# Optimization experiments

Hardware: AMD Instinct MI355X
Metric: run time of the kernel (lower is better)

The kernel has to match this reference:

```python
import jax, jax.numpy as jnp
import numpy as np

# ---- constants mirroring init_kwargs ----
S = 128          # sheet_units
KA = 25          # aff_cf_units
C = 2            # aff_cf_channels
KL = 25          # lat_cf_units
EXC = 9          # exc_units
DA = 1           # aff_cf_dilation
DL = 1           # lat_cf_dilation
HOMEO_TARGET = 0.04
STRENGTH = 1.0

# ---- radial helper masks (get_circle / get_radial_cos) ----
def _dist(n):
    g = jnp.arange(n, dtype=jnp.float32) - (n - 1) / 2.0
    return jnp.sqrt(g[:, None] ** 2 + g[None, :] ** 2)

def _circle(n, r):
    return (_dist(n) < r).astype(jnp.float32)

def _rcos(n, wl):
    return jnp.cos(_dist(n) * jnp.pi / wl)

# afferent envelope: [C*KA*KA], channel-major like torch repeat+view
_ae = _rcos(KA, KA) ** 2 * _circle(KA, KA / 2)
_ae = _ae / _ae.max()
AFF_ENV = jnp.tile(_ae.reshape(1, KA * KA), (C, 1)).reshape(C * KA * KA)

# lateral (LRI) envelope: [KL*KL]
_inh = _rcos(KL, EXC / DL) ** 2 * _circle(KL, EXC / (2 * DL))
_le = _rcos(KL, KL) ** 2 * (1.0 - _inh) * _circle(KL, KL / 2)
LRI_ENV = (_le / _le.max()).reshape(KL * KL)

def _unfold(x, k, dil):
    """x: [C,H,W] -> patches [L, C*k*k], torch F.unfold ordering (C slowest)."""
    Cc, H, W = x.shape
    out = H - dil * (k - 1)
    idx = jnp.arange(out)[:, None] + dil * jnp.arange(k)[None, :]  # [out,k]
    p = x[:, idx, :]          # [C,out,k,W]
    p = p[:, :, :, idx]       # [C,out,k,out,k]
    p = p.transpose(1, 3, 0, 2, 4)  # [out_i,out_j,C,ki,kj]
    return p.reshape(out * out, Cc * k * k)

def setup_inputs() -> dict:
    key = jax.random.key(0)
    k1, k2 = jax.random.split(key)
    in_size = S + DA * (KA - 1)  # 152
    x = jax.random.uniform(k1, (1, C, in_size, in_size), dtype=jnp.float32)
    rfs = jax.random.uniform(k2, (S * S, C * KA * KA, 1), dtype=jnp.float32)
    rfs = rfs / rfs.sum(1, keepdims=True)
    lat_weights = jnp.ones((S * S, KL * KL, 1), jnp.float32) / (KL * KL)
    adathresh = jnp.zeros((1, 1, S, S), jnp.float32)
    return {"x": x, "rfs": rfs, "lat_weights": lat_weights, "adathresh": adathresh}

def _forward(x, rfs, lat_weights, adathresh):
    relu = jax.nn.relu
    rfs = relu(rfs)                 # no_grad positive clamp of params
    lw = relu(lat_weights)
    # afferent: unfold + envelope + per-pixel dot (bmm with [L,F,1])
    tiles = _unfold(x[0], KA, DA) * AFF_ENV[None, :]          # [L, C*KA*KA]
    raw_aff = jnp.einsum('lf,lf->l', tiles, rfs[:, :, 0]).reshape(S, S)
    aff = jax.lax.stop_gradient(raw_aff) - adathresh[0, 0]
    lat = relu(aff)
    # lateral inhibition: pad so unfold yields S*S positions
    p = DL * (KL - 1) // 2
    lt = _unfold(jnp.pad(lat, p)[None], KL, DL) * LRI_ENV[None, :]  # [L, KL*KL]
    lat_neg = jnp.einsum('lf,lf->l', lt, jax.lax.stop_gradient(lw)[:, :, 0]).reshape(S, S)
    lat = lat - lat_neg
    lat = jnp.tanh(relu(lat * STRENGTH + aff))
    # hebbian lateral correlations term (learning_flag path)
    lt2 = _unfold(jnp.pad(lat, p, constant_values=HOMEO_TARGET)[None], KL, DL) * LRI_ENV[None, :]
    weighted = lt2 * lat.reshape(S * S, 1)
    lat_correlations = jnp.einsum('lf,lf->', weighted, lw[:, :, 0])
    return (raw_aff.reshape(1, 1, S, S), lat.reshape(1, 1, S, S),
            lat_correlations, tiles[:, None, :])

def reference(x, rfs, lat_weights, adathresh):
    return _forward(x, rfs, lat_weights, adathresh)
```

## Files before the change

kernel.cpp:

```cpp
#include <hip/hip_runtime.h>
#include <math.h>

#define S 128
#define KA 25
#define KL 25
#define PATCH 625
#define FEAT 1250
#define PI_F 3.14159265358979323846f
#define PADW 152
#define PADA (PADW * PADW)

#define WS_LRI 0
#define WS_AE 640
#define WS_LAT0P 1280
#define WS_LATFP 24384
#define WS_PART 47488
#define NPART 2048

__device__ __forceinline__ int div25(int r) { return (r * 10486) >> 18; }

__device__ __forceinline__ int woff(int r) { return r + 127 * div25(r); }

__global__ __launch_bounds__(256) void k_init(float* __restrict__ ws) {
    const int tid = threadIdx.x;
    if (blockIdx.x == 0) {
        __shared__ float s_tmp[640];
        __shared__ float s_red[4];
        for (int s = tid; s < 640; s += 256) {
            int q = s / 160;
            int t = s - q * 160;
            int r = (t << 2) | q;
            float v = 0.0f;
            if (r < PATCH) {
                float di = (float)div25(r) - 12.0f;
                float dj = (float)(r - 25 * div25(r)) - 12.0f;
                float d = sqrtf(di * di + dj * dj);
                if (d < 12.5f) {
                    float c = cosf(d * (PI_F / 25.0f));
                    v = c * c;
                }
            }
            ws[WS_AE + s] = v;
        }
        float m = 0.0f;
        for (int s = tid; s < 640; s += 256) {
            int q = s / 160;
            int t = s - q * 160;
            int r = (t << 2) | q;
            float v = 0.0f;
            if (r < PATCH) {
                float di = (float)div25(r) - 12.0f;
                float dj = (float)(r - 25 * div25(r)) - 12.0f;
                float d = sqrtf(di * di + dj * dj);
                if (d < 12.5f) {
                    float c1 = cosf(d * (PI_F / 25.0f));
                    float inh = 0.0f;
                    if (d < 4.5f) {
                        float c2 = cosf(d * (PI_F / 9.0f));
                        inh = c2 * c2;
                    }
                    v = c1 * c1 * (1.0f - inh);
                }
            }
            s_tmp[s] = v;
            m = fmaxf(m, v);
        }
        for (int o = 32; o; o >>= 1) m = fmaxf(m, __shfl_down(m, o));
        if (!(tid & 63)) s_red[tid >> 6] = m;
        __syncthreads();
        float inv = 1.0f / fmaxf(fmaxf(s_red[0], s_red[1]),
                                 fmaxf(s_red[2], s_red[3]));
        for (int s = tid; s < 640; s += 256) ws[WS_LRI + s] = s_tmp[s] * inv;
    }
    const int gid = blockIdx.x * 256 + tid;
    const int gsz = gridDim.x * 256;
    for (int i = gid; i < 2 * PADA; i += gsz) {
        if (i < PADA) ws[WS_LAT0P + i] = 0.0f;
        else          ws[WS_LATFP + i - PADA] = 0.04f;
    }
}

__global__ __launch_bounds__(256) void k_aff(const float* __restrict__ x,
                                             const float* __restrict__ rfs,
                                             const float* __restrict__ ada,
                                             float* __restrict__ raw_aff,
                                             float* __restrict__ ws) {
    __shared__ float s_ae[640];
    const int tid = threadIdx.x;
    for (int i = tid; i < 640; i += 256) s_ae[i] = ws[WS_AE + i];
    __syncthreads();

    const int lane = tid & 63;
    const int wid = blockIdx.x * 4 + (tid >> 6);

    for (int l = wid; l < S * S; l += 8192) {
        const int li = l >> 7, lj = l & 127;
        const int wbase = li * PADW + lj;
        const long base = (long)l * FEAT;
        const int peel = (l & 1) ? 2 : 0;

        float acc = 0.0f;
        if (lane < peel) {
            int f = lane;
            float t = x[wbase + f] * s_ae[(f & 3) * 160 + (f >> 2)];
            acc += t * fmaxf(rfs[base + f], 0.0f);
        }
        const int n4 = (FEAT - peel) >> 2;
        for (int k = lane; k < n4; k += 64) {
            int f0 = peel + (k << 2);
            const float4 rv = *reinterpret_cast<const float4*>(rfs + base + f0);
#pragma unroll
            for (int j = 0; j < 4; ++j) {
                int f = f0 + j;
                int c = (f >= PATCH);
                int r = f - (c ? PATCH : 0);
                float t = x[c * PADA + wbase + woff(r)]
                          * s_ae[(r & 3) * 160 + (r >> 2)];
                acc += t * fmaxf((&rv.x)[j], 0.0f);
            }
        }
        const int tail = (FEAT - peel) & 3;
        if (lane < tail) {
            int f = peel + (n4 << 2) + lane;
            int r = f - PATCH;
            float t = x[PADA + wbase + woff(r)] * s_ae[(r & 3) * 160 + (r >> 2)];
            acc += t * fmaxf(rfs[base + f], 0.0f);
        }

        for (int o = 32; o; o >>= 1) acc += __shfl_down(acc, o);
        if (!lane) {
            raw_aff[l] = acc;
            ws[WS_LAT0P + (li + 12) * PADW + (lj + 12)] =
                fmaxf(acc - ada[l], 0.0f);
        }
    }
}

#define NTILE 20480000
#define NF4 5119999
__global__ __launch_bounds__(256) void k_tiles(const float* __restrict__ x,
                                               float* __restrict__ tiles,
                                               const float* __restrict__ ws) {
    __shared__ float s_ae[640];
    const int tid = threadIdx.x;
    for (int i = tid; i < 640; i += 256) s_ae[i] = ws[WS_AE + i];
    __syncthreads();

    const int gid = blockIdx.x * 256 + tid;
    const int gsz = gridDim.x * 256;
    for (long k = gid; k < NF4; k += gsz) {
        long i0 = 3 + (k << 2);
        float4 v;
#pragma unroll
        for (int j = 0; j < 4; ++j) {
            unsigned int e = (unsigned int)(i0 + j);
            unsigned int l = e / 1250u;
            int f = (int)(e - l * 1250u);
            int c = (f >= PATCH);
            int r = f - (c ? PATCH : 0);
            int li = (int)(l >> 7), lj = (int)(l & 127u);
            (&v.x)[j] = x[c * PADA + li * PADW + lj + woff(r)]
                        * s_ae[(r & 3) * 160 + (r >> 2)];
        }
        *reinterpret_cast<float4*>(tiles + i0) = v;
    }
    if (blockIdx.x == 0 && tid < 4) {
        unsigned int e = (tid < 3) ? (unsigned int)tid : (NTILE - 1u);
        unsigned int l = e / 1250u;
        int f = (int)(e - l * 1250u);
        int c = (f >= PATCH);
        int r = f - (c ? PATCH : 0);
        int li = (int)(l >> 7), lj = (int)(l & 127u);
        tiles[e] = x[c * PADA + li * PADW + lj + woff(r)]
                   * s_ae[(r & 3) * 160 + (r >> 2)];
    }
}

__global__ __launch_bounds__(256) void k_lat(const float* __restrict__ raw_aff,
                                             const float* __restrict__ ada,
                                             const float* __restrict__ lw,
                                             float* __restrict__ latf,
                                             float* __restrict__ ws) {
    __shared__ float s_le[640];
    const int tid = threadIdx.x;
    for (int i = tid; i < 640; i += 256) s_le[i] = ws[WS_LRI + i];
    __syncthreads();

    const int lane = tid & 63;
    const int wid = blockIdx.x * 4 + (tid >> 6);
    const float* __restrict__ plat0 = ws + WS_LAT0P;

    for (int l = wid; l < S * S; l += 8192) {
        const int li = l >> 7, lj = l & 127;
        const int wbase = li * PADW + lj;
        const long base = (long)l * PATCH;

        float acc = 0.0f;
        const int peel = (4 - (l & 3)) & 3;
        if (lane < peel) {
            int f = lane;
            acc += plat0[wbase + f] * s_le[(f & 3) * 160 + (f >> 2)]
                   * fmaxf(lw[base + f], 0.0f);
        }
        const int n4 = (PATCH - peel) >> 2;
        for (int k = lane; k < n4; k += 64) {
            int f0 = peel + (k << 2);
            const float4 w4 = *reinterpret_cast<const float4*>(lw + base + f0);
#pragma unroll
            for (int j = 0; j < 4; ++j) {
                int f = f0 + j;
                acc += plat0[wbase + woff(f)] * s_le[(f & 3) * 160 + (f >> 2)]
                       * fmaxf((&w4.x)[j], 0.0f);
            }
        }
        const int tail = (PATCH - peel) & 3;
        if (lane < tail) {
            int f = peel + (n4 << 2) + lane;
            acc += plat0[wbase + woff(f)] * s_le[(f & 3) * 160 + (f >> 2)]
                   * fmaxf(lw[base + f], 0.0f);
        }
        for (int o = 32; o; o >>= 1) acc += __shfl_down(acc, o);

        if (!lane) {
            float aff_l = raw_aff[l] - ada[l];
            float lat0_l = fmaxf(aff_l, 0.0f);
            float v = (lat0_l - acc)  + aff_l;
            float lv = tanhf(fmaxf(v, 0.0f));
            latf[l] = lv;
            ws[WS_LATFP + (li + 12) * PADW + (lj + 12)] = lv;
        }
    }
}

__global__ __launch_bounds__(256) void k_corr(const float* __restrict__ latf,
                                              const float* __restrict__ lw,
                                              float* __restrict__ ws) {
    __shared__ float s_le[640];
    __shared__ float s_part[4];
    const int tid = threadIdx.x;
    for (int i = tid; i < 640; i += 256) s_le[i] = ws[WS_LRI + i];
    __syncthreads();

    const int lane = tid & 63, wv = tid >> 6;
    const int wid = blockIdx.x * 4 + wv;
    const float* __restrict__ platf = ws + WS_LATFP;

    float wsum = 0.0f;
    for (int l = wid; l < S * S; l += 8192) {
        const int li = l >> 7, lj = l & 127;
        const int wbase = li * PADW + lj;
        const long base = (long)l * PATCH;

        float acc = 0.0f;
        const int peel = (4 - (l & 3)) & 3;
        if (lane < peel) {
            int f = lane;
            acc += platf[wbase + f] * s_le[(f & 3) * 160 + (f >> 2)]
                   * fmaxf(lw[base + f], 0.0f);
        }
        const int n4 = (PATCH - peel) >> 2;
        for (int k = lane; k < n4; k += 64) {
            int f0 = peel + (k << 2);
            const float4 w4 = *reinterpret_cast<const float4*>(lw + base + f0);
#pragma unroll
            for (int j = 0; j < 4; ++j) {
                int f = f0 + j;
                acc += platf[wbase + woff(f)] * s_le[(f & 3) * 160 + (f >> 2)]
                       * fmaxf((&w4.x)[j], 0.0f);
            }
        }
        const int tail = (PATCH - peel) & 3;
        if (lane < tail) {
            int f = peel + (n4 << 2) + lane;
            acc += platf[wbase + woff(f)] * s_le[(f & 3) * 160 + (f >> 2)]
                   * fmaxf(lw[base + f], 0.0f);
        }
        for (int o = 32; o; o >>= 1) acc += __shfl_down(acc, o);
        if (!lane) wsum += acc * latf[l];
    }
    if (!lane) s_part[wv] = wsum;
    __syncthreads();
    if (!tid)
        ws[WS_PART + blockIdx.x] = s_part[0] + s_part[1] + s_part[2] + s_part[3];
}

__global__ __launch_bounds__(256) void k_reduce(const float* __restrict__ ws,
                                                float* __restrict__ corr) {
    __shared__ float s_part[4];
    const int tid = threadIdx.x;
    const int lane = tid & 63, wv = tid >> 6;
    float acc = 0.0f;
    for (int i = tid; i < NPART; i += 256) acc += ws[WS_PART + i];
    for (int o = 32; o; o >>= 1) acc += __shfl_down(acc, o);
    if (!lane) s_part[wv] = acc;
    __syncthreads();
    if (!tid) corr[0] = s_part[0] + s_part[1] + s_part[2] + s_part[3];
}

extern "C" void kernel_launch(void* const* d_in, const int* in_sizes, int n_in,
                              void* d_out, int out_size, void* d_ws, size_t ws_size,
                              hipStream_t stream) {
    const float* x   = (const float*)d_in[0];
    const float* rfs = (const float*)d_in[1];
    const float* lw  = (const float*)d_in[2];
    const float* ada = (const float*)d_in[3];

    float* out      = (float*)d_out;
    float* raw_aff  = out;
    float* latf     = out + S * S;
    float* corr     = out + 2 * S * S;
    float* tiles    = out + 2 * S * S + 1;
    float* ws       = (float*)d_ws;

    k_init<<<16, 256, 0, stream>>>(ws);
    k_aff<<<2048, 256, 0, stream>>>(x, rfs, ada, raw_aff, ws);
    k_tiles<<<2048, 256, 0, stream>>>(x, tiles, ws);
    k_lat<<<2048, 256, 0, stream>>>(raw_aff, ada, lw, latf, ws);
    k_corr<<<2048, 256, 0, stream>>>(latf, lw, ws);
    k_reduce<<<1, 256, 0, stream>>>(ws, corr);
}
```

Baseline: 232.5 us.

## Fuse afferent dot and tiles output, one pixel per wave with upfront loads

Merges the afferent dot-product kernel and the tiles-materialisation kernel, so each wave computes its pixel's patch values once, writes them to the tiles output, and accumulates the dot product. This removes a second pass that recomputed every gather of x and envelope multiply. The lateral and correlation kernels also drop their grid-stride loops: each wave handles exactly one pixel and issues all its weight float4 loads before consuming them, which raises memory-level parallelism. The grid doubles to 4096 blocks and the partial-sum count grows to match. Tile stores are now scalar per element rather than float4, which could cost some write efficiency.

```diff
diff --git a/kernel.cpp b/kernel.cpp
--- a/kernel.cpp
+++ b/kernel.cpp
@@ -3,7 +3,6 @@
 
 #define S 128
 #define KA 25
-#define KL 25
 #define PATCH 625
 #define FEAT 1250
 #define PI_F 3.14159265358979323846f
@@ -15,11 +14,11 @@
 #define WS_LAT0P 1280
 #define WS_LATFP 24384
 #define WS_PART 47488
-#define NPART 2048
+#define NPART 4096
 
 __device__ __forceinline__ int div25(int r) { return (r * 10486) >> 18; }
-
 __device__ __forceinline__ int woff(int r) { return r + 127 * div25(r); }
+__device__ __forceinline__ int eslot(int r) { return (r & 3) * 160 + (r >> 2); }
 
 __global__ __launch_bounds__(256) void k_init(float* __restrict__ ws) {
     const int tid = threadIdx.x;
@@ -27,8 +26,7 @@
         __shared__ float s_tmp[640];
         __shared__ float s_red[4];
         for (int s = tid; s < 640; s += 256) {
-            int q = s / 160;
-            int t = s - q * 160;
+            int q = s / 160, t = s - q * 160;
             int r = (t << 2) | q;
             float v = 0.0f;
             if (r < PATCH) {
@@ -44,8 +42,7 @@
         }
         float m = 0.0f;
         for (int s = tid; s < 640; s += 256) {
-            int q = s / 160;
-            int t = s - q * 160;
+            int q = s / 160, t = s - q * 160;
             int r = (t << 2) | q;
             float v = 0.0f;
             if (r < PATCH) {
@@ -80,99 +77,70 @@
     }
 }
 
-__global__ __launch_bounds__(256) void k_aff(const float* __restrict__ x,
-                                             const float* __restrict__ rfs,
-                                             const float* __restrict__ ada,
-                                             float* __restrict__ raw_aff,
-                                             float* __restrict__ ws) {
+__global__ __launch_bounds__(256) void k_afftiles(const float* __restrict__ x,
+                                                  const float* __restrict__ rfs,
+                                                  const float* __restrict__ ada,
+                                                  float* __restrict__ raw_aff,
+                                                  float* __restrict__ tiles,
+                                                  float* __restrict__ ws) {
     __shared__ float s_ae[640];
     const int tid = threadIdx.x;
     for (int i = tid; i < 640; i += 256) s_ae[i] = ws[WS_AE + i];
     __syncthreads();
 
     const int lane = tid & 63;
-    const int wid = blockIdx.x * 4 + (tid >> 6);
-
-    for (int l = wid; l < S * S; l += 8192) {
-        const int li = l >> 7, lj = l & 127;
-        const int wbase = li * PADW + lj;
-        const long base = (long)l * FEAT;
-        const int peel = (l & 1) ? 2 : 0;
-
-        float acc = 0.0f;
-        if (lane < peel) {
-            int f = lane;
-            float t = x[wbase + f] * s_ae[(f & 3) * 160 + (f >> 2)];
-            acc += t * fmaxf(rfs[base + f], 0.0f);
-        }
-        const int n4 = (FEAT - peel) >> 2;
-        for (int k = lane; k < n4; k += 64) {
-            int f0 = peel + (k << 2);
-            const float4 rv = *reinterpret_cast<const float4*>(rfs + base + f0);
-#pragma unroll
-            for (int j = 0; j < 4; ++j) {
-                int f = f0 + j;
-                int c = (f >= PATCH);
-                int r = f - (c ? PATCH : 0);
-                float t = x[c * PADA + wbase + woff(r)]
-                          * s_ae[(r & 3) * 160 + (r >> 2)];
-                acc += t * fmaxf((&rv.x)[j], 0.0f);
-            }
-        }
-        const int tail = (FEAT - peel) & 3;
-        if (lane < tail) {
-            int f = peel + (n4 << 2) + lane;
-            int r = f - PATCH;
-            float t = x[PADA + wbase + woff(r)] * s_ae[(r & 3) * 160 + (r >> 2)];
-            acc += t * fmaxf(rfs[base + f], 0.0f);
-        }
-
-        for (int o = 32; o; o >>= 1) acc += __shfl_down(acc, o);
-        if (!lane) {
-            raw_aff[l] = acc;
-            ws[WS_LAT0P + (li + 12) * PADW + (lj + 12)] =
-                fmaxf(acc - ada[l], 0.0f);
-        }
-    }
-}
-
-#define NTILE 20480000
-#define NF4 5119999
-__global__ __launch_bounds__(256) void k_tiles(const float* __restrict__ x,
-                                               float* __restrict__ tiles,
-                                               const float* __restrict__ ws) {
-    __shared__ float s_ae[640];
-    const int tid = threadIdx.x;
-    for (int i = tid; i < 640; i += 256) s_ae[i] = ws[WS_AE + i];
-    __syncthreads();
-
-    const int gid = blockIdx.x * 256 + tid;
-    const int gsz = gridDim.x * 256;
-    for (long k = gid; k < NF4; k += gsz) {
-        long i0 = 3 + (k << 2);
-        float4 v;
+    const int l = blockIdx.x * 4 + (tid >> 6);
+    const int li = l >> 7, lj = l & 127;
+    const int wb = li * PADW + lj;
+    const long B = (long)l * FEAT;
+    const int peel = (l & 1) ? 2 : 0;
+
+    float acc = 0.0f;
+    if (lane < peel) {
+        int f = lane;
+        float t = x[wb + f] * s_ae[eslot(f)];
+        tiles[B + f] = t;
+        acc += t * fmaxf(rfs[B + f], 0.0f);
+    }
+
+    const float* __restrict__ rb = rfs + B + peel;
+    const float4 rv0 = *reinterpret_cast<const float4*>(rb + 4 * lane);
+    const float4 rv1 = *reinterpret_cast<const float4*>(rb + 4 * (lane + 64));
+    const float4 rv2 = *reinterpret_cast<const float4*>(rb + 4 * (lane + 128));
+    const float4 rv3 = *reinterpret_cast<const float4*>(rb + 4 * (lane + 192));
+    float4 rv4 = {0.0f, 0.0f, 0.0f, 0.0f};
+    if (lane < 56) rv4 = *reinterpret_cast<const float4*>(rb + 4 * (lane + 256));
+
+    auto consume = [&](const float4& rv, int k) {
+        const int f0 = peel + 4 * k;
 #pragma unroll
         for (int j = 0; j < 4; ++j) {
-            unsigned int e = (unsigned int)(i0 + j);
-            unsigned int l = e / 1250u;
-            int f = (int)(e - l * 1250u);
-            int c = (f >= PATCH);
-            int r = f - (c ? PATCH : 0);
-            int li = (int)(l >> 7), lj = (int)(l & 127u);
-            (&v.x)[j] = x[c * PADA + li * PADW + lj + woff(r)]
-                        * s_ae[(r & 3) * 160 + (r >> 2)];
-        }
-        *reinterpret_cast<float4*>(tiles + i0) = v;
-    }
-    if (blockIdx.x == 0 && tid < 4) {
-        unsigned int e = (tid < 3) ? (unsigned int)tid : (NTILE - 1u);
-        unsigned int l = e / 1250u;
-        int f = (int)(e - l * 1250u);
-        int c = (f >= PATCH);
-        int r = f - (c ? PATCH : 0);
-        int li = (int)(l >> 7), lj = (int)(l & 127u);
-        tiles[e] = x[c * PADA + li * PADW + lj + woff(r)]
-                   * s_ae[(r & 3) * 160 + (r >> 2)];
+            int f = f0 + j;
+            int c = (f >= PATCH) ? 1 : 0;
+            int r = f - c * PATCH;
+            float t = x[c * PADA + wb + woff(r)] * s_ae[eslot(r)];
+            tiles[B + f] = t;
+            acc += t * fmaxf((&rv.x)[j], 0.0f);
+        }
+    };
+    consume(rv0, lane);
+    consume(rv1, lane + 64);
+    consume(rv2, lane + 128);
+    consume(rv3, lane + 192);
+    if (lane < 56) consume(rv4, lane + 256);
+
+    if (lane < 2 - peel) {
+        int f = 1248 + lane;
+        int r = f - PATCH;
+        float t = x[PADA + wb + woff(r)] * s_ae[eslot(r)];
+        tiles[B + f] = t;
+        acc += t * fmaxf(rfs[B + f], 0.0f);
+    }
+
+    for (int o = 32; o; o >>= 1) acc += __shfl_down(acc, o);
+    if (!lane) {
+        raw_aff[l] = acc;
+        ws[WS_LAT0P + (li + 12) * PADW + (lj + 12)] = fmaxf(acc - ada[l], 0.0f);
     }
 }
 
@@ -187,48 +155,51 @@
     __syncthreads();
 
     const int lane = tid & 63;
-    const int wid = blockIdx.x * 4 + (tid >> 6);
+    const int l = blockIdx.x * 4 + (tid >> 6);
+    const int li = l >> 7, lj = l & 127;
+    const int wb = li * PADW + lj;
+    const long B = (long)l * PATCH;
+    const int peel = (4 - (l & 3)) & 3;
+    const int n4 = (PATCH - peel) >> 2;
+    const int tail = (PATCH - peel) & 3;
     const float* __restrict__ plat0 = ws + WS_LAT0P;
 
-    for (int l = wid; l < S * S; l += 8192) {
-        const int li = l >> 7, lj = l & 127;
-        const int wbase = li * PADW + lj;
-        const long base = (long)l * PATCH;
-
-        float acc = 0.0f;
-        const int peel = (4 - (l & 3)) & 3;
-        if (lane < peel) {
-            int f = lane;
-            acc += plat0[wbase + f] * s_le[(f & 3) * 160 + (f >> 2)]
-                   * fmaxf(lw[base + f], 0.0f);
-        }
-        const int n4 = (PATCH - peel) >> 2;
-        for (int k = lane; k < n4; k += 64) {
-            int f0 = peel + (k << 2);
-            const float4 w4 = *reinterpret_cast<const float4*>(lw + base + f0);
+    float acc = 0.0f;
+    if (lane < peel) {
+        int f = lane;
+        acc += plat0[wb + f] * s_le[eslot(f)] * fmaxf(lw[B + f], 0.0f);
+    }
+    const float* __restrict__ wbp = lw + B + peel;
+    const float4 w0 = *reinterpret_cast<const float4*>(wbp + 4 * lane);
+    const float4 w1 = *reinterpret_cast<const float4*>(wbp + 4 * (lane + 64));
+    const int rem = n4 - 128;
+    float4 w2 = {0.0f, 0.0f, 0.0f, 0.0f};
+    if (lane < rem) w2 = *reinterpret_cast<const float4*>(wbp + 4 * (lane + 128));
+
+    auto consume = [&](const float4& w, int k) {
+        const int f0 = peel + 4 * k;
 #pragma unroll
-            for (int j = 0; j < 4; ++j) {
-                int f = f0 + j;
-                acc += plat0[wbase + woff(f)] * s_le[(f & 3) * 160 + (f >> 2)]
-                       * fmaxf((&w4.x)[j], 0.0f);
-            }
-        }
-        const int tail = (PATCH - peel) & 3;
-        if (lane < tail) {
-            int f = peel + (n4 << 2) + lane;
-            acc += plat0[wbase + woff(f)] * s_le[(f & 3) * 160 + (f >> 2)]
-                   * fmaxf(lw[base + f], 0.0f);
-        }
-        for (int o = 32; o; o >>= 1) acc += __shfl_down(acc, o);
-
-        if (!lane) {
-            float aff_l = raw_aff[l] - ada[l];
-            float lat0_l = fmaxf(aff_l, 0.0f);
-            float v = (lat0_l - acc)  + aff_l;
-            float lv = tanhf(fmaxf(v, 0.0f));
-            latf[l] = lv;
-            ws[WS_LATFP + (li + 12) * PADW + (lj + 12)] = lv;
-        }
+        for (int j = 0; j < 4; ++j) {
+            int f = f0 + j;
+            acc += plat0[wb + woff(f)] * s_le[eslot(f)] * fmaxf((&w.x)[j], 0.0f);
+        }
+    };
+    consume(w0, lane);
+    consume(w1, lane + 64);
+    if (lane < rem) consume(w2, lane + 128);
+    if (lane < tail) {
+        int f = peel + 4 * n4 + lane;
+        acc += plat0[wb + woff(f)] * s_le[eslot(f)] * fmaxf(lw[B + f], 0.0f);
+    }
+    for (int o = 32; o; o >>= 1) acc += __shfl_down(acc, o);
+
+    if (!lane) {
+        float aff_l = raw_aff[l] - ada[l];
+        float lat0_l = fmaxf(aff_l, 0.0f);
+        float v = (lat0_l - acc)  + aff_l;
+        float lv = tanhf(fmaxf(v, 0.0f));
+        latf[l] = lv;
+        ws[WS_LATFP + (li + 12) * PADW + (lj + 12)] = lv;
     }
 }
 
@@ -236,65 +207,67 @@
                                               const float* __restrict__ lw,
                                               float* __restrict__ ws) {
     __shared__ float s_le[640];
-    __shared__ float s_part[4];
+    __shared__ float s_red[4];
     const int tid = threadIdx.x;
     for (int i = tid; i < 640; i += 256) s_le[i] = ws[WS_LRI + i];
     __syncthreads();
 
     const int lane = tid & 63, wv = tid >> 6;
-    const int wid = blockIdx.x * 4 + wv;
+    const int l = blockIdx.x * 4 + wv;
+    const int li = l >> 7, lj = l & 127;
+    const int wb = li * PADW + lj;
+    const long B = (long)l * PATCH;
+    const int peel = (4 - (l & 3)) & 3;
+    const int n4 = (PATCH - peel) >> 2;
+    const int tail = (PATCH - peel) & 3;
     const float* __restrict__ platf = ws + WS_LATFP;
 
-    float wsum = 0.0f;
-    for (int l = wid; l < S * S; l += 8192) {
-        const int li = l >> 7, lj = l & 127;
-        const int wbase = li * PADW + lj;
-        const long base = (long)l * PATCH;
-
-        float acc = 0.0f;
-        const int peel = (4 - (l & 3)) & 3;
-        if (lane < peel) {
-            int f = lane;
-            acc += platf[wbase + f] * s_le[(f & 3) * 160 + (f >> 2)]
-                   * fmaxf(lw[base + f], 0.0f);
-        }
-        const int n4 = (PATCH - peel) >> 2;
-        for (int k = lane; k < n4; k += 64) {
-            int f0 = peel + (k << 2);
-            const float4 w4 = *reinterpret_cast<const float4*>(lw + base + f0);
+    float acc = 0.0f;
+    if (lane < peel) {
+        int f = lane;
+        acc += platf[wb + f] * s_le[eslot(f)] * fmaxf(lw[B + f], 0.0f);
+    }
+    const float* __restrict__ wbp = lw + B + peel;
+    const float4 w0 = *reinterpret_cast<const float4*>(wbp + 4 * lane);
+    const float4 w1 = *reinterpret_cast<const float4*>(wbp + 4 * (lane + 64));
+    const int rem = n4 - 128;
+    float4 w2 = {0.0f, 0.0f, 0.0f, 0.0f};
+    if (lane < rem) w2 = *reinterpret_cast<const float4*>(wbp + 4 * (lane + 128));
+
+    auto consume = [&](const float4& w, int k) {
+        const int f0 = peel + 4 * k;
 #pragma unroll
-            for (int j = 0; j < 4; ++j) {
-                int f = f0 + j;
-                acc += platf[wbase + woff(f)] * s_le[(f & 3) * 160 + (f >> 2)]
-                       * fmaxf((&w4.x)[j], 0.0f);
-            }
-        }
-        const int tail = (PATCH - peel) & 3;
-        if (lane < tail) {
-            int f = peel + (n4 << 2) + lane;
-            acc += platf[wbase + woff(f)] * s_le[(f & 3) * 160 + (f >> 2)]
-                   * fmaxf(lw[base + f], 0.0f);
-        }
-        for (int o = 32; o; o >>= 1) acc += __shfl_down(acc, o);
-        if (!lane) wsum += acc * latf[l];
-    }
-    if (!lane) s_part[wv] = wsum;
+        for (int j = 0; j < 4; ++j) {
+            int f = f0 + j;
+            acc += platf[wb + woff(f)] * s_le[eslot(f)] * fmaxf((&w.x)[j], 0.0f);
+        }
+    };
+    consume(w0, lane);
+    consume(w1, lane + 64);
+    if (lane < rem) consume(w2, lane + 128);
+    if (lane < tail) {
+        int f = peel + 4 * n4 + lane;
+        acc += platf[wb + woff(f)] * s_le[eslot(f)] * fmaxf(lw[B + f], 0.0f);
+    }
+    for (int o = 32; o; o >>= 1) acc += __shfl_down(acc, o);
+
+    if (!lane) s_red[wv] = acc * latf[l];
     __syncthreads();
     if (!tid)
-        ws[WS_PART + blockIdx.x] = s_part[0] + s_part[1] + s_part[2] + s_part[3];
+        ws[WS_PART + blockIdx.x] = s_red[0] + s_red[1] + s_red[2] + s_red[3];
 }
 
 __global__ __launch_bounds__(256) void k_reduce(const float* __restrict__ ws,
                                                 float* __restrict__ corr) {
-    __shared__ float s_part[4];
+    __shared__ float s_red[4];
     const int tid = threadIdx.x;
     const int lane = tid & 63, wv = tid >> 6;
     float acc = 0.0f;
     for (int i = tid; i < NPART; i += 256) acc += ws[WS_PART + i];
     for (int o = 32; o; o >>= 1) acc += __shfl_down(acc, o);
-    if (!lane) s_part[wv] = acc;
-    __syncthreads();
-    if (!tid) corr[0] = s_part[0] + s_part[1] + s_part[2] + s_part[3];
+    if (!lane) s_red[wv] = acc;
+    __syncthreads();
+    if (!tid) corr[0] = s_red[0] + s_red[1] + s_red[2] + s_red[3];
 }
 
 extern "C" void kernel_launch(void* const* d_in, const int* in_sizes, int n_in,
@@ -313,9 +286,8 @@
     float* ws       = (float*)d_ws;
 
     k_init<<<16, 256, 0, stream>>>(ws);
-    k_aff<<<2048, 256, 0, stream>>>(x, rfs, ada, raw_aff, ws);
-    k_tiles<<<2048, 256, 0, stream>>>(x, tiles, ws);
-    k_lat<<<2048, 256, 0, stream>>>(raw_aff, ada, lw, latf, ws);
-    k_corr<<<2048, 256, 0, stream>>>(latf, lw, ws);
+    k_afftiles<<<4096, 256, 0, stream>>>(x, rfs, ada, raw_aff, tiles, ws);
+    k_lat<<<4096, 256, 0, stream>>>(raw_aff, ada, lw, latf, ws);
+    k_corr<<<4096, 256, 0, stream>>>(latf, lw, ws);
     k_reduce<<<1, 256, 0, stream>>>(ws, corr);
 }
```

Result: faster. 227.3 us (-2.3%).
